# Kernel optimization log

Hardware: AMD Instinct MI355X
Metric: run time of the kernel (lower is better)

## Reference

```python
import jax, jax.numpy as jnp
import numpy as np

H = 16          # num_attention_heads
MAX_REL = 512   # max_relative_positions


def setup_inputs() -> dict:
    key = jax.random.key(0)
    ks = jax.random.split(key, 6)
    B, N, Hid = 4, 1024, 1024
    s = 0.02
    hidden_states = jax.random.normal(ks[0], (B, N, Hid), jnp.float32)
    attention_mask = jnp.ones((B, N, N), jnp.bool_)
    ids = jnp.arange(N, dtype=jnp.int32)
    relative_pos = (ids[:, None] - ids[None, :])[None]                      # [1,N,N]
    rel_embeddings = jax.random.normal(ks[1], (2 * MAX_REL, Hid), jnp.float32)
    in_proj_w = jax.random.normal(ks[2], (3 * Hid, Hid), jnp.float32) * s
    q_bias = jnp.zeros((Hid,), jnp.float32)
    v_bias = jnp.zeros((Hid,), jnp.float32)
    pos_proj_w = jax.random.normal(ks[3], (Hid, Hid), jnp.float32) * s
    pos_q_proj_w = jax.random.normal(ks[4], (Hid, Hid), jnp.float32) * s
    pos_q_proj_b = jnp.zeros((Hid,), jnp.float32)
    return {"hidden_states": hidden_states, "attention_mask": attention_mask,
            "relative_pos": relative_pos, "rel_embeddings": rel_embeddings,
            "in_proj_w": in_proj_w, "q_bias": q_bias, "v_bias": v_bias,
            "pos_proj_w": pos_proj_w, "pos_q_proj_w": pos_q_proj_w,
            "pos_q_proj_b": pos_q_proj_b}


def reference(hidden_states, attention_mask, relative_pos, rel_embeddings,
              in_proj_w, q_bias, v_bias, pos_proj_w, pos_q_proj_w, pos_q_proj_b):
    B, N, Hid = hidden_states.shape
    D = Hid // H
    scale_factor = 3                                  # 1 + len([c2p, p2c])
    scale = jnp.sqrt(jnp.asarray(D * scale_factor, jnp.float32))

    # fused in_proj, split to per-head q/k/v (torch view order: [B,N,H,3D])
    qkv = (hidden_states @ in_proj_w.T).reshape(B, N, H, 3 * D).transpose(0, 2, 1, 3)
    q, k, v = jnp.split(qkv, 3, axis=-1)              # each [B,H,N,D]
    q = (q + q_bias.reshape(1, H, 1, D)) / scale
    v = v + v_bias.reshape(1, H, 1, D)

    scores = jnp.einsum('bhqd,bhkd->bhqk', q, k)      # [B,H,N,N]

    # ---- disentangled c2p / p2c bias ----
    span = min(N, MAX_REL)                            # attention span (static)
    rel = rel_embeddings[MAX_REL - span: MAX_REL + span]   # [2*span, Hid]
    rp = relative_pos[:, None]                        # [1,1,N,N] int

    # content -> position
    pos_k = (rel @ pos_proj_w.T).reshape(2 * span, H, D).transpose(1, 0, 2)   # [H,2s,D]
    c2p = jnp.einsum('bhqd,hsd->bhqs', q, pos_k)                              # [B,H,N,2s]
    c2p_idx = jnp.clip(rp + span, 0, 2 * span - 1)
    c2p = jnp.take_along_axis(c2p, jnp.broadcast_to(c2p_idx, (B, H, N, N)), axis=-1)

    # position -> content (pos query scaled by same sqrt(d*scale_factor))
    pos_q = ((rel @ pos_q_proj_w.T + pos_q_proj_b)
             .reshape(2 * span, H, D).transpose(1, 0, 2)) / scale             # [H,2s,D]
    p2c = jnp.einsum('bhkd,hsd->bhks', k, pos_q)                              # [B,H,N,2s]
    p2c_idx = jnp.clip(-rp + span, 0, 2 * span - 1)
    p2c = jnp.take_along_axis(p2c, jnp.broadcast_to(p2c_idx, (B, H, N, N)), axis=-1)
    p2c = p2c.swapaxes(-1, -2)                        # transpose(-1,-2)

    scores = scores + c2p + p2c

    neg = jnp.finfo(scores.dtype).min
    scores = jnp.where(attention_mask[:, None], scores, neg)
    probs = jax.nn.softmax(scores, axis=-1)
    ctx = jnp.einsum('bhqk,bhkd->bhqd', probs, v)
    return ctx.transpose(0, 2, 1, 3).reshape(B, N, Hid)
```

## Files before the change

kernel.cpp:

```cpp
#include <hip/hip_runtime.h>
#include <hip/hip_bf16.h>
#include <stdint.h>

typedef __bf16 bf16;
typedef __bf16 bf16x2 __attribute__((ext_vector_type(2)));
typedef __bf16 bf16x4 __attribute__((ext_vector_type(4)));
typedef __bf16 bf16x8 __attribute__((ext_vector_type(8)));
typedef float  f32x4  __attribute__((ext_vector_type(4)));

#define MFMA16(A_, B_, C_) __builtin_amdgcn_mfma_f32_16x16x32_bf16((A_), (B_), (C_), 0, 0, 0)
#define GLOAD_LDS16(G_, L_) __builtin_amdgcn_global_load_lds( \
    (const __attribute__((address_space(1))) void*)(G_),      \
    (__attribute__((address_space(3))) void*)(L_), 16, 0, 0)

static constexpr float INV_SCALE = 0.07216878364870322992f;

__global__ void conv_all(const float* __restrict__ s0, const float* __restrict__ s1,
                         const float* __restrict__ s2, const float* __restrict__ s3,
                         const float* __restrict__ s4,
                         bf16* __restrict__ d0, bf16* __restrict__ d1,
                         bf16* __restrict__ d2, bf16* __restrict__ d3,
                         bf16* __restrict__ d4) {
  int i = blockIdx.x * blockDim.x + threadIdx.x;
  const float* s; bf16* d; int j;
  if      (i <  524288) { s = s0; d = d0; j = i; }
  else if (i <  917504) { s = s1; d = d1; j = i -  524288; }
  else if (i < 1048576) { s = s2; d = d2; j = i -  917504; }
  else if (i < 1179648) { s = s3; d = d3; j = i - 1048576; }
  else                  { s = s4; d = d4; j = i - 1179648; }
  const float4* p = (const float4*)s + (size_t)j * 2;
  float4 a = p[0], b = p[1];
  bf16x8 o;
  o[0] = (bf16)a.x; o[1] = (bf16)a.y; o[2] = (bf16)a.z; o[3] = (bf16)a.w;
  o[4] = (bf16)b.x; o[5] = (bf16)b.y; o[6] = (bf16)b.z; o[7] = (bf16)b.w;
  *((bf16x8*)d + j) = o;
}

__global__ __launch_bounds__(256)
void gemm_all(const bf16* __restrict__ hs, const bf16* __restrict__ wq,
              const bf16* __restrict__ rel, const bf16* __restrict__ wpk,
              const bf16* __restrict__ wpq,
              bf16* __restrict__ q_buf, bf16* __restrict__ k_buf,
              bf16* __restrict__ vt_buf, bf16* __restrict__ posk,
              bf16* __restrict__ posq,
              const float* __restrict__ qb, const float* __restrict__ vb,
              const float* __restrict__ pqb)
{
  __shared__ bf16 As[128 * 32];
  __shared__ bf16 Bs[128 * 32];
  const int tid = threadIdx.x;
  const int w = tid >> 6, l = tid & 63;
  const int wr = w >> 1, wc = w & 1;
  const int kg = l >> 4, li = l & 15;

  const int bid = blockIdx.x;
  int mode, bm, bn;
  const bf16 *A, *B;
  if (bid < 768) { mode = 0; bm = (bid & 31) * 128; bn = (bid >> 5) * 128; A = hs; B = wq; }
  else {
    int pb = bid - 768;
    mode = 1 + (pb >> 6);
    bm = (pb & 7) * 128; bn = ((pb >> 3) & 7) * 128;
    A = rel; B = (mode == 1) ? wpk : wpq;
  }

  const int lrow = l >> 2;
  const int lcol = (l & 3) * 8;

  f32x4 acc[4][4] = {};

  for (int k0 = 0; k0 < 1024; k0 += 32) {
    if (k0) __syncthreads();
    #pragma unroll
    for (int i = 0; i < 2; i++) {
      int r = w * 32 + i * 16 + lrow;
      GLOAD_LDS16(A + (size_t)(bm + r) * 1024 + k0 + lcol, As + (w * 32 + i * 16) * 32);
      GLOAD_LDS16(B + (size_t)(bn + r) * 1024 + k0 + lcol, Bs + (w * 32 + i * 16) * 32);
    }
    __syncthreads();
    bf16x8 af[4], bfr[4];
    #pragma unroll
    for (int m = 0; m < 4; m++)
      af[m] = *(const bf16x8*)&As[(wr * 64 + m * 16 + li) * 32 + kg * 8];
    #pragma unroll
    for (int n = 0; n < 4; n++)
      bfr[n] = *(const bf16x8*)&Bs[(wc * 64 + n * 16 + li) * 32 + kg * 8];
    #pragma unroll
    for (int m = 0; m < 4; m++)
      #pragma unroll
      for (int n = 0; n < 4; n++)
        acc[m][n] = MFMA16(af[m], bfr[n], acc[m][n]);
  }

  #pragma unroll
  for (int m = 0; m < 4; m++) {
    #pragma unroll
    for (int n = 0; n < 4; n++) {
      #pragma unroll
      for (int r = 0; r < 4; r++) {
        int i = bm + wr * 64 + m * 16 + kg * 4 + r;
        int j = bn + wc * 64 + n * 16 + li;
        float v = acc[m][n][r];
        if (mode == 0) {
          int b = i >> 10, nn = i & 1023;
          int h = j / 192, c = j - h * 192;
          if (c < 64) {
            v = (v + qb[h * 64 + c]) * INV_SCALE;
            q_buf[(size_t)((b * 16 + h) * 1024 + nn) * 64 + c] = (bf16)v;
          } else if (c < 128) {
            k_buf[(size_t)((b * 16 + h) * 1024 + nn) * 64 + (c - 64)] = (bf16)v;
          } else {
            v += vb[h * 64 + (c - 128)];
            vt_buf[(size_t)((b * 16 + h) * 64 + (c - 128)) * 1024 + nn] = (bf16)v;
          }
        } else {
          if (mode == 2) v = (v + pqb[j]) * INV_SCALE;
          bf16* op = (mode == 1) ? posk : posq;
          op[(size_t)((j >> 6) * 1024 + i) * 64 + (j & 63)] = (bf16)v;
        }
      }
    }
  }
}

__global__ __launch_bounds__(512, 4)
void attn_fused(const bf16* __restrict__ q_buf, const bf16* __restrict__ k_buf,
                const bf16* __restrict__ vt_buf, const bf16* __restrict__ posk,
                const bf16* __restrict__ posq, float* __restrict__ out)
{
  __shared__ __align__(16) bf16 Kt[64 * 64];
  __shared__ __align__(16) bf16 Vt[64 * 64];
  __shared__ __align__(16) bf16 ring2[128 * 130];
  __shared__ __align__(16) bf16 band[64 * 196];

  const int tid = threadIdx.x, w = tid >> 6, l = tid & 63;
  const int kg = l >> 4, li = l & 15;

  const int lin = blockIdx.y * 8 + blockIdx.x;
  const int xcd = lin & 7, idx = lin >> 3;
  const int bh = ((idx >> 3) << 3) | xcd;
  const int qt = idx & 7;

  const int b = bh >> 4, h = bh & 15;
  const int q0 = qt * 128;
  const int qw = q0 + w * 16;

  const bf16* qp = q_buf + ((size_t)bh * 1024 + qw) * 64;
  const bf16* kp = k_buf + (size_t)bh * 65536;
  const bf16* vp = vt_buf + (size_t)bh * 65536;
  const bf16* pk = posk + (size_t)h * 65536;
  const bf16* pq = posq + (size_t)h * 65536;

  bf16x8 aq[2];
  #pragma unroll
  for (int kk = 0; kk < 2; kk++)
    aq[kk] = *(const bf16x8*)(qp + li * 64 + kk * 32 + kg * 8);

  float l_r[4] = {0.f, 0.f, 0.f, 0.f};
  f32x4 o_acc[4] = {};

  const int J0 = qw + 528;

  auto ring_fill = [&](int lo) {
    bf16x8 bp_[4][2];
    #pragma unroll
    for (int n = 0; n < 4; n++) {
      int j = lo + 16 * n + li;
      int jc = j < 0 ? 0 : (j > 1023 ? 1023 : j);
      #pragma unroll
      for (int kk = 0; kk < 2; kk++)
        bp_[n][kk] = *(const bf16x8*)(pk + (size_t)jc * 64 + kk * 32 + kg * 8);
    }
    #pragma unroll
    for (int n = 0; n < 4; n++) {
      f32x4 c = {};
      c = MFMA16(aq[0], bp_[n][0], c);
      c = MFMA16(aq[1], bp_[n][1], c);
      #pragma unroll
      for (int r = 0; r < 4; r++) {
        int rowf = ((lo + 16 * n + li) - (qw + kg * 4 + r)) & 127;
        ring2[rowf * 130 + w * 16 + kg * 4 + r] = (bf16)c[r];
      }
    }
  };

  ring_fill(J0 - 64);

  for (int t = 0; t < 16; t++) {
    const int k0 = t * 64;
    __syncthreads();

    {
      int srow = tid >> 3;
      int su = (tid & 7) ^ (srow & 7);
      GLOAD_LDS16(kp + (size_t)(k0 + srow) * 64 + su * 8,  Kt + (w << 9));
      GLOAD_LDS16(vp + (size_t)srow * 1024 + k0 + su * 8,  Vt + (w << 9));
    }
    ring_fill(J0 - 64 * (t + 2));
    __syncthreads();

    f32x4 sa[4] = {};
    #pragma unroll
    for (int kk = 0; kk < 2; kk++) {
      int g = kk * 4 + kg;
      #pragma unroll
      for (int n = 0; n < 4; n++) {
        int row = 16 * n + li;
        bf16x8 kB = *(const bf16x8*)&Kt[row * 64 + ((g ^ (row & 7)) * 8)];
        sa[n] = MFMA16(aq[kk], kB, sa[n]);
      }
    }
    {
      const int i0 = q0 - k0 + 449;
      const int mW = w & 3;
      const int rowA = 16 * mW + li;
      bf16x8 kA[2];
      #pragma unroll
      for (int kk = 0; kk < 2; kk++)
        kA[kk] = *(const bf16x8*)&Kt[rowA * 64 + (((kk * 4 + kg) ^ (rowA & 7)) * 8)];
      const int ctb = (w >> 2) * 6;
      #pragma unroll
      for (int h3 = 0; h3 < 2; h3++) {
        bf16x8 qB[3][2];
        #pragma unroll
        for (int c3 = 0; c3 < 3; c3++) {
          int ct = ctb + h3 * 3 + c3;
          int i = i0 + ct * 16 + li;
          int ic = i < 0 ? 0 : (i > 1023 ? 1023 : i);
          #pragma unroll
          for (int kk = 0; kk < 2; kk++)
            qB[c3][kk] = *(const bf16x8*)(pq + (size_t)ic * 64 + kk * 32 + kg * 8);
        }
        #pragma unroll
        for (int c3 = 0; c3 < 3; c3++) {
          int ct = ctb + h3 * 3 + c3;
          f32x4 pca = {};
          pca = MFMA16(kA[0], qB[c3][0], pca);
          pca = MFMA16(kA[1], qB[c3][1], pca);
          int colc = ct * 16 + li;
          #pragma unroll
          for (int r = 0; r < 4; r++)
            band[(16 * mW + kg * 4 + r) * 196 + colc + r + 1] = (bf16)pca[r];
        }
      }
    }
    __syncthreads();

    float pe[4][4];
    #pragma unroll
    for (int n = 0; n < 4; n++) {
      int kl = 16 * n + li;
      int rowr = (512 - (k0 + kl)) & 127;
      const bf16* rbase = &ring2[rowr * 130 + w * 16 + kg * 4];
      bf16x2 ra = *(const bf16x2*)rbase;
      bf16x2 rb = *(const bf16x2*)(rbase + 2);
      int c0s = w * 16 + kg * 4 - kl + 63 + (li & 3) + 1;
      bf16x4 bb = *(const bf16x4*)&band[kl * 196 + c0s];
      pe[n][0] = __expf(sa[n][0] + (float)ra[0] + (float)bb[0]);
      pe[n][1] = __expf(sa[n][1] + (float)ra[1] + (float)bb[1]);
      pe[n][2] = __expf(sa[n][2] + (float)rb[0] + (float)bb[2]);
      pe[n][3] = __expf(sa[n][3] + (float)rb[1] + (float)bb[3]);
      l_r[0] += pe[n][0];
      l_r[1] += pe[n][1];
      l_r[2] += pe[n][2];
      l_r[3] += pe[n][3];
    }
    bf16* plw = Kt + (w << 9);
    #pragma unroll
    for (int ck = 0; ck < 2; ck++) {
      #pragma unroll
      for (int n2 = 0; n2 < 2; n2++) {
        #pragma unroll
        for (int r = 0; r < 4; r++) {
          int q = kg * 4 + r;
          int kpr = n2 * 16 + li;
          int phys = (kpr >> 3) ^ ((q >> 1) & 3);
          plw[q * 32 + phys * 8 + (kpr & 7)] = (bf16)pe[ck * 2 + n2][r];
        }
      }
      bf16x8 pA = *(const bf16x8*)&plw[li * 32 + ((kg ^ ((li >> 1) & 3)) * 8)];
      #pragma unroll
      for (int n = 0; n < 4; n++) {
        int row = 16 * n + li;
        bf16x8 vB = *(const bf16x8*)&Vt[row * 64 + (((ck * 4 + kg) ^ (row & 7)) * 8)];
        o_acc[n] = MFMA16(pA, vB, o_acc[n]);
      }
    }
  }

  #pragma unroll
  for (int r = 0; r < 4; r++)
    #pragma unroll
    for (int d = 1; d < 16; d <<= 1)
      l_r[r] += __shfl_xor(l_r[r], d);
  #pragma unroll
  for (int n = 0; n < 4; n++)
    #pragma unroll
    for (int r = 0; r < 4; r++)
      out[((size_t)(b * 1024 + qw + kg * 4 + r)) * 1024 + h * 64 + 16 * n + li] =
          o_acc[n][r] / l_r[r];
}

extern "C" void kernel_launch(void* const* d_in, const int* in_sizes, int n_in,
                              void* d_out, int out_size, void* d_ws, size_t ws_size,
                              hipStream_t stream)
{
  (void)in_sizes; (void)n_in; (void)out_size;
  const float* hs   = (const float*)d_in[0];
  const float* rel  = (const float*)d_in[3];
  const float* wqkv = (const float*)d_in[4];
  const float* qb   = (const float*)d_in[5];
  const float* vb   = (const float*)d_in[6];
  const float* wpk  = (const float*)d_in[7];
  const float* wpq  = (const float*)d_in[8];
  const float* pqb  = (const float*)d_in[9];
  float* out = (float*)d_out;
  char* ws = (char*)d_ws;

  size_t off = 0;
  auto alloc = [&](size_t elems) { bf16* p = (bf16*)(ws + off); off += elems * 2; return p; };
  bf16* hs_b   = alloc((size_t)4 << 20);
  bf16* wq_b   = alloc((size_t)3 << 20);
  bf16* rel_b  = alloc((size_t)1 << 20);
  bf16* wpk_b  = alloc((size_t)1 << 20);
  bf16* wpq_b  = alloc((size_t)1 << 20);
  bf16* q_buf  = alloc((size_t)4 << 20);
  bf16* k_buf  = alloc((size_t)4 << 20);
  bf16* vt_buf = alloc((size_t)4 << 20);
  bf16* posk   = alloc((size_t)1 << 20);
  bf16* posq   = alloc((size_t)1 << 20);
  if (ws_size < off) return;

  conv_all<<<5120, 256, 0, stream>>>(hs, wqkv, rel, wpk, wpq,
                                     hs_b, wq_b, rel_b, wpk_b, wpq_b);

  gemm_all<<<896, 256, 0, stream>>>(hs_b, wq_b, rel_b, wpk_b, wpq_b,
                                    q_buf, k_buf, vt_buf, posk, posq,
                                    qb, vb, pqb);

  attn_fused<<<dim3(8, 64), 512, 0, stream>>>(
      q_buf, k_buf, vt_buf, posk, posq, out);
}
```

Measured before the change: 244.3 us.

## Double-buffer K tiles in LDS and load V fragments directly into registers

The single K/V LDS staging is replaced by a two-slot K buffer. The next K tile is prefetched with global_load_lds while the current tile is used, which removes one barrier per iteration. V fragments for the PV MFMA are now read straight from global memory into registers instead of going through LDS, and the probability staging reuses the current K slot after an extra barrier. This aims to hide K load latency and cut LDS traffic. The cost is strided global V loads per lane, and it relies on the async LDS load having completed by the next iteration's barrier.

Measured after the change: 304.4 us. +24.6%, slower.

```diff
diff --git a/kernel.cpp b/kernel.cpp
--- a/kernel.cpp
+++ b/kernel.cpp
@@ -128,8 +128,7 @@
                 const bf16* __restrict__ vt_buf, const bf16* __restrict__ posk,
                 const bf16* __restrict__ posq, float* __restrict__ out)
 {
-  __shared__ __align__(16) bf16 Kt[64 * 64];
-  __shared__ __align__(16) bf16 Vt[64 * 64];
+  __shared__ __align__(16) bf16 KtBuf[2][64 * 64];
   __shared__ __align__(16) bf16 ring2[128 * 130];
   __shared__ __align__(16) bf16 band[64 * 196];
 
@@ -184,20 +183,23 @@
     }
   };
 
+  const int srow = tid >> 3;
+  const int su = (tid & 7) ^ (srow & 7);
+
+  GLOAD_LDS16(kp + (size_t)srow * 64 + su * 8, &KtBuf[0][w << 9]);
   ring_fill(J0 - 64);
 
   for (int t = 0; t < 16; t++) {
     const int k0 = t * 64;
+    const int cur = t & 1;
+    const bf16* Kt = KtBuf[cur];
+
     __syncthreads();
 
-    {
-      int srow = tid >> 3;
-      int su = (tid & 7) ^ (srow & 7);
-      GLOAD_LDS16(kp + (size_t)(k0 + srow) * 64 + su * 8,  Kt + (w << 9));
-      GLOAD_LDS16(vp + (size_t)srow * 1024 + k0 + su * 8,  Vt + (w << 9));
-    }
+    if (t < 15)
+      GLOAD_LDS16(kp + (size_t)(k0 + 64 + srow) * 64 + su * 8, &KtBuf[cur ^ 1][w << 9]);
+
     ring_fill(J0 - 64 * (t + 2));
-    __syncthreads();
 
     f32x4 sa[4] = {};
     #pragma unroll
@@ -246,6 +248,13 @@
     }
     __syncthreads();
 
+    bf16x8 vB[2][4];
+    #pragma unroll
+    for (int ck = 0; ck < 2; ck++)
+      #pragma unroll
+      for (int n = 0; n < 4; n++)
+        vB[ck][n] = *(const bf16x8*)(vp + (size_t)(16 * n + li) * 1024 + k0 + ck * 32 + kg * 8);
+
     float pe[4][4];
     #pragma unroll
     for (int n = 0; n < 4; n++) {
@@ -265,7 +274,9 @@
       l_r[2] += pe[n][2];
       l_r[3] += pe[n][3];
     }
-    bf16* plw = Kt + (w << 9);
+    __syncthreads();
+
+    bf16* plw = &KtBuf[cur][w << 9];
     #pragma unroll
     for (int ck = 0; ck < 2; ck++) {
       #pragma unroll
@@ -280,11 +291,8 @@
       }
       bf16x8 pA = *(const bf16x8*)&plw[li * 32 + ((kg ^ ((li >> 1) & 3)) * 8)];
       #pragma unroll
-      for (int n = 0; n < 4; n++) {
-        int row = 16 * n + li;
-        bf16x8 vB = *(const bf16x8*)&Vt[row * 64 + (((ck * 4 + kg) ^ (row & 7)) * 8)];
-        o_acc[n] = MFMA16(pA, vB, o_acc[n]);
-      }
+      for (int n = 0; n < 4; n++)
+        o_acc[n] = MFMA16(pA, vB[ck][n], o_acc[n]);
     }
   }
 
```
